# Kernel optimization log

Hardware: AMD Instinct MI355X
Metric: run time of the kernel (lower is better)

The kernel has to match this reference:

```python
import jax, jax.numpy as jnp
import numpy as np

B, T, C, H = 4, 2048, 1024, 16
HS = C // H  # head_size = 64
FF = 4 * C   # 4096
EPS = 1e-5


def _layernorm(x, g, b):
    mu = jnp.mean(x, axis=-1, keepdims=True)
    var = jnp.mean(jnp.square(x - mu), axis=-1, keepdims=True)
    return (x - mu) * jax.lax.rsqrt(var + EPS) * g + b


def setup_inputs() -> dict:
    key = jax.random.key(0)
    ks = jax.random.split(key, 12)
    s_in = 1.0 / np.sqrt(C)
    s_ff = 1.0 / np.sqrt(FF)
    return {
        "x": jax.random.normal(ks[0], (B, T, C), jnp.float32),
        # per-head projection weights stacked: [H, C, HS]
        "Wq": jax.random.normal(ks[1], (H, C, HS), jnp.float32) * s_in,
        "Wk": jax.random.normal(ks[2], (H, C, HS), jnp.float32) * s_in,
        "Wv": jax.random.normal(ks[3], (H, C, HS), jnp.float32) * s_in,
        "Wo": jax.random.normal(ks[4], (C, C), jnp.float32) * s_in,
        "bo": jnp.zeros((C,), jnp.float32),
        "g1": jnp.ones((C,), jnp.float32),
        "b1": jnp.zeros((C,), jnp.float32),
        "g2": jnp.ones((C,), jnp.float32),
        "b2": jnp.zeros((C,), jnp.float32),
        "W1": jax.random.normal(ks[5], (C, FF), jnp.float32) * s_in,
        "bf1": jnp.zeros((FF,), jnp.float32),
        "W2": jax.random.normal(ks[6], (FF, C), jnp.float32) * s_ff,
        "bf2": jnp.zeros((C,), jnp.float32),
    }


def reference(x, Wq, Wk, Wv, Wo, bo, g1, b1, g2, b2, W1, bf1, W2, bf2):
    # pre-norm
    h = _layernorm(x, g1, b1)                       # [B,T,C]
    q = jnp.einsum('btc,hcd->bhtd', h, Wq)          # [B,H,T,HS]
    k = jnp.einsum('btc,hcd->bhtd', h, Wk)
    v = jnp.einsum('btc,hcd->bhtd', h, Wv)
    w = jnp.einsum('bhtd,bhsd->bhts', q, k) * (HS ** -0.5)  # [B,H,T,S]
    mask = jnp.tril(jnp.ones((T, T), bool))          # causal tril
    w = jnp.where(mask[None, None], w, -jnp.inf)
    # NB: original code softmaxes over dim=1 of [B,T,T], i.e. the QUERY axis
    w = jax.nn.softmax(w, axis=-2)
    o = jnp.einsum('bhts,bhsd->bhtd', w, v)          # [B,H,T,HS]
    o = jnp.transpose(o, (0, 2, 1, 3)).reshape(B, T, C)  # concat heads
    x = x + o @ Wo + bo                              # residual 1 (dropout=0)
    f = _layernorm(x, g2, b2)
    ff = jax.nn.relu(f @ W1 + bf1) @ W2 + bf2        # FFN (dropout=0)
    return x + ff
```

## Files before the change

kernel.cpp:

```cpp
#include <hip/hip_runtime.h>
#include <hip/hip_bf16.h>


#define T_SEQ 2048
#define SCALE2 0.1803368801f

typedef __attribute__((ext_vector_type(8))) short short8;
typedef __attribute__((ext_vector_type(4))) float f32x4;

typedef __attribute__((address_space(1))) unsigned int g_u32;
typedef __attribute__((address_space(3))) unsigned int l_u32;

__device__ __forceinline__ unsigned short f2bf(float f) {
  __hip_bfloat16 h = __float2bfloat16(f);
  union { __hip_bfloat16 h; unsigned short u; } x; x.h = h;
  return x.u;
}
__device__ __forceinline__ float bf2f(unsigned short u) {
  union { unsigned u; float f; } x; x.u = (unsigned)u << 16;
  return x.f;
}

__device__ __forceinline__ void g2lds16(const void* g, void* l) {
  __builtin_amdgcn_global_load_lds((g_u32*)g, (l_u32*)l, 16, 0, 0);
}

__device__ __forceinline__ int xcd_swz(int flat, int nwg) {
  if ((nwg & 7) != 0) return flat;
  return (flat & 7) * (nwg >> 3) + (flat >> 3);
}

template <int EPI, int BN>
__global__ __launch_bounds__(512, 2) void gemm256(
    const unsigned short* __restrict__ A, const unsigned short* __restrict__ Bt,
    int M, int N, int K,
    unsigned short* __restrict__ out16, float* __restrict__ outF,
    const float* __restrict__ bias, const float* __restrict__ resid) {
  constexpr int WN = BN / 4;
  constexpr int FN = WN / 16;
  extern __shared__ unsigned short lds[];
  unsigned short* ldsA = lds;
  unsigned short* ldsB = lds + 2 * 16384;
  const int tid = threadIdx.x, lane = tid & 63, wid = tid >> 6;
  const int wm = wid >> 2, wn = wid & 3;
  const int nx = gridDim.x;
  const int flat = blockIdx.y * nx + blockIdx.x;
  const int swz = xcd_swz(flat, nx * gridDim.y);
  const int mBase = (swz / nx) * 256, nBase = (swz % nx) * BN;

  f32x4 acc[8][FN];
#pragma unroll
  for (int i = 0; i < 8; ++i)
#pragma unroll
    for (int j = 0; j < FN; ++j)
#pragma unroll
      for (int e = 0; e < 4; ++e) acc[i][j][e] = 0.f;

  auto stage = [&](int buf, int kt) {
    const int k0 = kt << 6;
#pragma unroll
    for (int it = 0; it < 4; ++it) {
      int g = it * 512 + tid;
      int row = g >> 3, colL = g & 7;
      int col = colL ^ (row & 7);
      g2lds16(A + ((size_t)(mBase + row) * K + k0 + col * 8),
              &ldsA[buf * 16384 + (it * 512 + wid * 64) * 8]);
    }
#pragma unroll
    for (int it = 0; it < (BN * 8) / 512; ++it) {
      int g = it * 512 + tid;
      int row = g >> 3, colL = g & 7;
      int col = colL ^ (row & 7);
      g2lds16(Bt + ((size_t)(nBase + row) * K + k0 + col * 8),
              &ldsB[buf * (BN * 64) + (it * 512 + wid * 64) * 8]);
    }
  };

  const int nKT = K >> 6;
  stage(0, 0);
  __syncthreads();
  int cur = 0;
  for (int kt = 0; kt < nKT; ++kt) {
    if (kt + 1 < nKT) stage(cur ^ 1, kt + 1);

    short8 bf[FN][2];
#pragma unroll
    for (int fn = 0; fn < FN; ++fn)
#pragma unroll
      for (int ks = 0; ks < 2; ++ks) {
        int r = wn * WN + fn * 16 + (lane & 15);
        int c = (ks * 4 + (lane >> 4)) ^ (r & 7);
        bf[fn][ks] = *(const short8*)&ldsB[cur * (BN * 64) + r * 64 + c * 8];
      }
#pragma unroll
    for (int q = 0; q < 4; ++q) {
      short8 af[2][2];
#pragma unroll
      for (int mf = 0; mf < 2; ++mf)
#pragma unroll
        for (int ks = 0; ks < 2; ++ks) {
          int r = wm * 128 + q * 32 + mf * 16 + (lane & 15);
          int c = (ks * 4 + (lane >> 4)) ^ (r & 7);
          af[mf][ks] = *(const short8*)&ldsA[cur * 16384 + r * 64 + c * 8];
        }
      __builtin_amdgcn_s_setprio(1);
#pragma unroll
      for (int mf = 0; mf < 2; ++mf)
#pragma unroll
        for (int fn = 0; fn < FN; ++fn)
#pragma unroll
          for (int ks = 0; ks < 2; ++ks)
            acc[q * 2 + mf][fn] = __builtin_amdgcn_mfma_f32_16x16x32_bf16(
                af[mf][ks], bf[fn][ks], acc[q * 2 + mf][fn], 0, 0, 0);
      __builtin_amdgcn_s_setprio(0);
    }
    __syncthreads();
    cur ^= 1;
  }

#pragma unroll
  for (int am = 0; am < 8; ++am)
#pragma unroll
    for (int fn = 0; fn < FN; ++fn) {
      int col = nBase + wn * WN + fn * 16 + (lane & 15);
      int row0 = mBase + wm * 128 + am * 16 + ((lane >> 4) << 2);
      if (EPI == 0) {
#pragma unroll
        for (int r = 0; r < 4; ++r)
          out16[(size_t)(row0 + r) * N + col] = f2bf(acc[am][fn][r]);
      } else if (EPI == 1) {
        float bv = bias[col];
#pragma unroll
        for (int r = 0; r < 4; ++r) {
          size_t idx = (size_t)(row0 + r) * N + col;
          outF[idx] = acc[am][fn][r] + bv + resid[idx];
        }
      } else {
        float bv = bias[col];
#pragma unroll
        for (int r = 0; r < 4; ++r)
          out16[(size_t)(row0 + r) * N + col] =
              f2bf(fmaxf(acc[am][fn][r] + bv, 0.f));
      }
    }
}

__global__ __launch_bounds__(256) void ln_bf16(
    const float* __restrict__ x, const float* __restrict__ gw,
    const float* __restrict__ bw, unsigned short* __restrict__ out) {
  __shared__ float red[8];
  const int row = blockIdx.x, tid = threadIdx.x;
  const float4 v = ((const float4*)(x + (size_t)row * 1024))[tid];
  float s = v.x + v.y + v.z + v.w;
  float q = v.x * v.x + v.y * v.y + v.z * v.z + v.w * v.w;
#pragma unroll
  for (int off = 32; off >= 1; off >>= 1) {
    s += __shfl_down(s, off);
    q += __shfl_down(q, off);
  }
  const int lane = tid & 63, wid = tid >> 6;
  if (lane == 0) { red[wid] = s; red[4 + wid] = q; }
  __syncthreads();
  float S = red[0] + red[1] + red[2] + red[3];
  float Q = red[4] + red[5] + red[6] + red[7];
  float mu = S * (1.f / 1024.f);
  float var = Q * (1.f / 1024.f) - mu * mu;
  float rs = rsqrtf(var + 1e-5f);
  int c = tid * 4;
  ushort4 ov;
  ov.x = f2bf((v.x - mu) * rs * gw[c + 0] + bw[c + 0]);
  ov.y = f2bf((v.y - mu) * rs * gw[c + 1] + bw[c + 1]);
  ov.z = f2bf((v.z - mu) * rs * gw[c + 2] + bw[c + 2]);
  ov.w = f2bf((v.w - mu) * rs * gw[c + 3] + bw[c + 3]);
  *(ushort4*)&out[(size_t)row * 1024 + c] = ov;
}

__global__ __launch_bounds__(256) void pack_qkv(
    const float* __restrict__ Wq, const float* __restrict__ Wk,
    const float* __restrict__ Wv, unsigned short* __restrict__ out) {
  __shared__ float tile[64 * 65];
  const int tid = threadIdx.x;
  const float* W = (blockIdx.z == 0) ? Wq : (blockIdx.z == 1) ? Wk : Wv;
  const int h = blockIdx.y, r0 = blockIdx.x * 64;
#pragma unroll
  for (int it = 0; it < 4; ++it) {
    int e4 = it * 256 + tid;
    int r = e4 >> 4, c4 = e4 & 15;
    float4 v = *(const float4*)&W[((size_t)h * 1024 + r0 + r) * 64 + c4 * 4];
    tile[r * 65 + c4 * 4 + 0] = v.x;
    tile[r * 65 + c4 * 4 + 1] = v.y;
    tile[r * 65 + c4 * 4 + 2] = v.z;
    tile[r * 65 + c4 * 4 + 3] = v.w;
  }
  __syncthreads();
#pragma unroll
  for (int it = 0; it < 4; ++it) {
    int e4 = it * 256 + tid;
    int d = e4 >> 4, r4 = e4 & 15;
    ushort4 ov;
    ov.x = f2bf(tile[(r4 * 4 + 0) * 65 + d]);
    ov.y = f2bf(tile[(r4 * 4 + 1) * 65 + d]);
    ov.z = f2bf(tile[(r4 * 4 + 2) * 65 + d]);
    ov.w = f2bf(tile[(r4 * 4 + 3) * 65 + d]);
    *(ushort4*)&out[(size_t)(blockIdx.z * 1024 + h * 64 + d) * 1024 + r0 +
                    r4 * 4] = ov;
  }
}

__global__ __launch_bounds__(256) void transpose_cast(
    const float* __restrict__ in, unsigned short* __restrict__ out, int R,
    int C) {
  __shared__ float tile[64 * 65];
  const int tid = threadIdx.x;
  const int r0 = blockIdx.x * 64, c0 = blockIdx.y * 64;
#pragma unroll
  for (int it = 0; it < 4; ++it) {
    int e4 = it * 256 + tid;
    int r = e4 >> 4, c4 = e4 & 15;
    float4 v = *(const float4*)&in[(size_t)(r0 + r) * C + c0 + c4 * 4];
    tile[r * 65 + c4 * 4 + 0] = v.x;
    tile[r * 65 + c4 * 4 + 1] = v.y;
    tile[r * 65 + c4 * 4 + 2] = v.z;
    tile[r * 65 + c4 * 4 + 3] = v.w;
  }
  __syncthreads();
#pragma unroll
  for (int it = 0; it < 4; ++it) {
    int e4 = it * 256 + tid;
    int c = e4 >> 4, r4 = e4 & 15;
    ushort4 ov;
    ov.x = f2bf(tile[(r4 * 4 + 0) * 65 + c]);
    ov.y = f2bf(tile[(r4 * 4 + 1) * 65 + c]);
    ov.z = f2bf(tile[(r4 * 4 + 2) * 65 + c]);
    ov.w = f2bf(tile[(r4 * 4 + 3) * 65 + c]);
    *(ushort4*)&out[(size_t)(c0 + c) * R + r0 + r4 * 4] = ov;
  }
}

__global__ __launch_bounds__(256) void vtrans(
    const unsigned short* __restrict__ qkv, const float* __restrict__ lpart,
    unsigned short* __restrict__ vT) {
  __shared__ unsigned short tile[64 * 66];
  const int tid = threadIdx.x;
  const int bh = blockIdx.y, b = bh >> 4, h = bh & 15;
  const int t0 = blockIdx.x * 64;
#pragma unroll
  for (int it = 0; it < 8; ++it) {
    int e2 = it * 256 + tid;
    int r = e2 >> 5, c2 = e2 & 31;
    unsigned v = *(const unsigned*)&qkv[(size_t)(b * T_SEQ + t0 + r) * 3072 +
                                        2048 + h * 64 + c2 * 2];
    float l0 = lpart[(size_t)bh * T_SEQ + t0 + r];
    float l1 = lpart[(size_t)(64 + bh) * T_SEQ + t0 + r];
    float li = 1.f / (l0 + l1);
    unsigned short lo = f2bf(bf2f((unsigned short)(v & 0xffff)) * li);
    unsigned short hi = f2bf(bf2f((unsigned short)(v >> 16)) * li);
    *(unsigned*)&tile[r * 66 + c2 * 2] = (unsigned)lo | ((unsigned)hi << 16);
  }
  __syncthreads();
#pragma unroll
  for (int it = 0; it < 8; ++it) {
    int e2 = it * 256 + tid;
    int d = e2 >> 5, t2 = e2 & 31;
    unsigned short a = tile[(t2 * 2) * 66 + d];
    unsigned short bb = tile[(t2 * 2 + 1) * 66 + d];
    unsigned pk = (unsigned)a | ((unsigned)bb << 16);
    *(unsigned*)&vT[(size_t)(bh * 64 + d) * T_SEQ + t0 + t2 * 2] = pk;
  }
}

__global__ __launch_bounds__(256, 4) void attn_stats(
    const unsigned short* __restrict__ qkv, float* __restrict__ lpart) {
  __shared__ unsigned short qt[4][2][32 * 64];
  __shared__ float redL[4][2][64];
  const int tid = threadIdx.x, lane = tid & 63, w = tid >> 6;
  const int f = xcd_swz(blockIdx.y * 32 + blockIdx.x, 2048);
  const int half = f & 1, px = (f >> 1) & 15, bh = f >> 5;
  const int b = bh >> 4, h = bh & 15;
  const int sxA = px, sxB = 31 - px;
  const int sA = sxA * 64, sB = sxB * 64;
  const int m = half * 4 + w;

  short8 kfA[4][2], kfB[4][2];
#pragma unroll
  for (int fn = 0; fn < 4; ++fn)
#pragma unroll
    for (int ks = 0; ks < 2; ++ks) {
      int d = 1024 + h * 64 + ks * 32 + ((lane >> 4) << 3);
      kfA[fn][ks] = *(const short8*)&qkv[(size_t)(b * T_SEQ + sA + fn * 16 +
                                                  (lane & 15)) * 3072 + d];
      kfB[fn][ks] = *(const short8*)&qkv[(size_t)(b * T_SEQ + sB + fn * 16 +
                                                  (lane & 15)) * 3072 + d];
    }
  float lA[4] = {0.f, 0.f, 0.f, 0.f}, lB[4] = {0.f, 0.f, 0.f, 0.f};

  auto stageQ = [&](int buf, int idx) {
    int t0 = idx * 32;
#pragma unroll
    for (int it = 0; it < 4; ++it) {
      int g = it * 64 + lane;
      int row = g >> 3;
      int col = (g & 7) ^ (row & 7);
      g2lds16(qkv + ((size_t)(b * T_SEQ + t0 + row) * 3072 + h * 64 + col * 8),
              &qt[w][buf][it * 512]);
    }
  };

  auto accum = [&](const short8 (&af)[2], const short8 (&kf)[4][2],
                   float (&lacc)[4], int sBase, int tRow, bool diag) {
    f32x4 sc[4];
#pragma unroll
    for (int fn = 0; fn < 4; ++fn)
#pragma unroll
      for (int e = 0; e < 4; ++e) sc[fn][e] = 0.f;
    __builtin_amdgcn_s_setprio(1);
#pragma unroll
    for (int fn = 0; fn < 4; ++fn)
#pragma unroll
      for (int ks = 0; ks < 2; ++ks)
        sc[fn] = __builtin_amdgcn_mfma_f32_16x16x32_bf16(af[ks], kf[fn][ks],
                                                         sc[fn], 0, 0, 0);
    __builtin_amdgcn_s_setprio(0);
    if (diag) {
#pragma unroll
      for (int fn = 0; fn < 4; ++fn) {
        int s = sBase + fn * 16 + (lane & 15);
        float e0 = (tRow + 0 >= s) ? exp2f(sc[fn][0] * SCALE2) : 0.f;
        float e1 = (tRow + 1 >= s) ? exp2f(sc[fn][1] * SCALE2) : 0.f;
        float e2 = (tRow + 2 >= s) ? exp2f(sc[fn][2] * SCALE2) : 0.f;
        float e3 = (tRow + 3 >= s) ? exp2f(sc[fn][3] * SCALE2) : 0.f;
        lacc[fn] += (e0 + e1) + (e2 + e3);
      }
    } else {
#pragma unroll
      for (int fn = 0; fn < 4; ++fn) {
        float e0 = exp2f(sc[fn][0] * SCALE2);
        float e1 = exp2f(sc[fn][1] * SCALE2);
        float e2 = exp2f(sc[fn][2] * SCALE2);
        float e3 = exp2f(sc[fn][3] * SCALE2);
        lacc[fn] += (e0 + e1) + (e2 + e3);
      }
    }
  };

  const int d0 = 2 * sxA - m;
  const int fi = m + (d0 > 0 ? (((d0 + 7) >> 3) << 3) : 0);
  int cur = 0;
  if (fi < 64) stageQ(0, fi);
  for (int idx = fi; idx < 64; idx += 8, cur ^= 1) {
    if (idx + 8 < 64) {
      stageQ(cur ^ 1, idx + 8);
      asm volatile("s_waitcnt vmcnt(4)" ::: "memory");
    } else {
      asm volatile("s_waitcnt vmcnt(0)" ::: "memory");
    }
    const int t0g = idx * 32;
    const bool doB = idx >= 2 * sxB;
#pragma unroll
    for (int mf = 0; mf < 2; ++mf) {
      short8 af[2];
#pragma unroll
      for (int ks = 0; ks < 2; ++ks) {
        int r = mf * 16 + (lane & 15);
        int c = (ks * 4 + (lane >> 4)) ^ (r & 7);
        af[ks] = *(const short8*)&qt[w][cur][r * 64 + c * 8];
      }
      int tRow = t0g + mf * 16 + ((lane >> 4) << 2);
      accum(af, kfA, lA, sA, tRow, idx <= 2 * sxA + 1);
      if (doB) accum(af, kfB, lB, sB, tRow, idx <= 2 * sxB + 1);
    }
  }
#pragma unroll
  for (int fn = 0; fn < 4; ++fn) {
    lA[fn] += __shfl_down(lA[fn], 32);
    lA[fn] += __shfl_down(lA[fn], 16);
    lB[fn] += __shfl_down(lB[fn], 32);
    lB[fn] += __shfl_down(lB[fn], 16);
  }
  if (lane < 16) {
#pragma unroll
    for (int fn = 0; fn < 4; ++fn) {
      redL[w][0][fn * 16 + lane] = lA[fn];
      redL[w][1][fn * 16 + lane] = lB[fn];
    }
  }
  __syncthreads();
  if (tid < 128) {
    int which = tid >> 6;
    float l = redL[0][which][lane] + redL[1][which][lane] +
              redL[2][which][lane] + redL[3][which][lane];
    int sbase = (which == 0) ? sA : sB;
    lpart[((size_t)half * 64 + bh) * T_SEQ + sbase + lane] = l;
  }
}

__global__ __launch_bounds__(256, 2) void attn_pv(
    const unsigned short* __restrict__ qkv, const unsigned short* __restrict__ vT,
    unsigned short* __restrict__ o) {
  __shared__ unsigned short kbuf[2][64 * 64];
  __shared__ unsigned short vbuf[2][64 * 64];
  __shared__ unsigned short pl[256 * 64];
  const int tid = threadIdx.x, lane = tid & 63, wid = tid >> 6;
  const int f = xcd_swz(blockIdx.y * 8 + blockIdx.x, 512);
  const int bx = f & 7, bh = f >> 3;
  const int b = bh >> 4, h = bh & 15;
  const int tA = bx * 128, tB = (15 - bx) * 128;
  const int nSTA = 2 * bx + 2, nSTB = 32 - 2 * bx;

  short8 qfA[2][2], qfB[2][2];
#pragma unroll
  for (int mf = 0; mf < 2; ++mf)
#pragma unroll
    for (int ks = 0; ks < 2; ++ks) {
      int d = h * 64 + ks * 32 + ((lane >> 4) << 3);
      int rloc = wid * 32 + mf * 16 + (lane & 15);
      qfA[mf][ks] =
          *(const short8*)&qkv[(size_t)(b * T_SEQ + tA + rloc) * 3072 + d];
      qfB[mf][ks] =
          *(const short8*)&qkv[(size_t)(b * T_SEQ + tB + rloc) * 3072 + d];
    }
  f32x4 oaccA[2][4], oaccB[2][4];
#pragma unroll
  for (int i = 0; i < 2; ++i)
#pragma unroll
    for (int j = 0; j < 4; ++j)
#pragma unroll
      for (int e = 0; e < 4; ++e) { oaccA[i][j][e] = 0.f; oaccB[i][j][e] = 0.f; }

  auto stage = [&](int buf, int st) {
#pragma unroll
    for (int it = 0; it < 2; ++it) {
      int g = it * 256 + tid;
      int row = g >> 3, colL = g & 7;
      int col = colL ^ (row & 7);
      g2lds16(qkv + ((size_t)(b * T_SEQ + st * 64 + row) * 3072 + 1024 +
                     h * 64 + col * 8),
              &kbuf[buf][(it * 256 + wid * 64) * 8]);
      g2lds16(vT + ((size_t)(bh * 64 + row) * T_SEQ + st * 64 + col * 8),
              &vbuf[buf][(it * 256 + wid * 64) * 8]);
    }
  };

  auto qkstore = [&](const short8 (&qf)[2][2], int rowBase, int tBase, int s0,
                     bool maskNeeded, int cur) {
    f32x4 sc[2][4];
#pragma unroll
    for (int i = 0; i < 2; ++i)
#pragma unroll
      for (int j = 0; j < 4; ++j)
#pragma unroll
        for (int e = 0; e < 4; ++e) sc[i][j][e] = 0.f;
    __builtin_amdgcn_s_setprio(1);
#pragma unroll
    for (int fn = 0; fn < 4; ++fn)
#pragma unroll
      for (int ks = 0; ks < 2; ++ks) {
        int r = fn * 16 + (lane & 15);
        int c = (ks * 4 + (lane >> 4)) ^ (r & 7);
        short8 kfr = *(const short8*)&kbuf[cur][r * 64 + c * 8];
        sc[0][fn] = __builtin_amdgcn_mfma_f32_16x16x32_bf16(qf[0][ks], kfr,
                                                            sc[0][fn], 0, 0, 0);
        sc[1][fn] = __builtin_amdgcn_mfma_f32_16x16x32_bf16(qf[1][ks], kfr,
                                                            sc[1][fn], 0, 0, 0);
      }
    __builtin_amdgcn_s_setprio(0);
#pragma unroll
    for (int fn = 0; fn < 4; ++fn) {
      int sg = s0 + fn * 16 + (lane & 15);
      int colb = (fn * 16 + (lane & 15)) * 2;
#pragma unroll
      for (int mf = 0; mf < 2; ++mf) {
        int rowB = rowBase + wid * 32 + mf * 16 + ((lane >> 4) << 2);
        int tRow = tBase + wid * 32 + mf * 16 + ((lane >> 4) << 2);
#pragma unroll
        for (int r = 0; r < 4; ++r) {
          float p = exp2f(sc[mf][fn][r] * SCALE2);
          if (maskNeeded) p = (tRow + r >= sg) ? p : 0.f;
          int row = rowB + r;
          int byteoff = row * 128 + (colb ^ ((row & 7) << 4));
          *(unsigned short*)((char*)pl + byteoff) = f2bf(p);
        }
      }
    }
  };

  stage(0, 0);
  int cur = 0;
  __syncthreads();

  for (int st = 0; st < nSTB; ++st) {
    const int s0 = st * 64;
    const bool doA = st < nSTA;

    if (doA) qkstore(qfA, 0, tA, s0, st >= nSTA - 2, cur);
    qkstore(qfB, 128, tB, s0, st >= nSTB - 2, cur);
    __syncthreads();

    if (st + 1 < nSTB) stage(cur ^ 1, st + 1);

    __builtin_amdgcn_s_setprio(1);
#pragma unroll
    for (int ks = 0; ks < 2; ++ks) {
      short8 paA[2], paB[2];
#pragma unroll
      for (int mf = 0; mf < 2; ++mf) {
        int rowa = wid * 32 + mf * 16 + (lane & 15);
        int kb = ks * 64 + ((lane >> 4) << 4);
        paB[mf] = *(const short8*)((const char*)pl + (128 + rowa) * 128 +
                                   (kb ^ ((rowa & 7) << 4)));
        if (doA)
          paA[mf] = *(const short8*)((const char*)pl + rowa * 128 +
                                     (kb ^ ((rowa & 7) << 4)));
      }
#pragma unroll
      for (int df = 0; df < 4; ++df) {
        int r = df * 16 + (lane & 15);
        int c = (ks * 4 + (lane >> 4)) ^ (r & 7);
        short8 vb = *(const short8*)&vbuf[cur][r * 64 + c * 8];
        oaccB[0][df] = __builtin_amdgcn_mfma_f32_16x16x32_bf16(paB[0], vb,
                                                               oaccB[0][df], 0, 0, 0);
        oaccB[1][df] = __builtin_amdgcn_mfma_f32_16x16x32_bf16(paB[1], vb,
                                                               oaccB[1][df], 0, 0, 0);
        if (doA) {
          oaccA[0][df] = __builtin_amdgcn_mfma_f32_16x16x32_bf16(paA[0], vb,
                                                                 oaccA[0][df], 0, 0, 0);
          oaccA[1][df] = __builtin_amdgcn_mfma_f32_16x16x32_bf16(paA[1], vb,
                                                                 oaccA[1][df], 0, 0, 0);
        }
      }
    }
    __builtin_amdgcn_s_setprio(0);
    __syncthreads();
    cur ^= 1;
  }
#pragma unroll
  for (int mf = 0; mf < 2; ++mf)
#pragma unroll
    for (int df = 0; df < 4; ++df) {
      int d = h * 64 + df * 16 + (lane & 15);
      int ra = tA + wid * 32 + mf * 16 + ((lane >> 4) << 2);
      int rb = tB + wid * 32 + mf * 16 + ((lane >> 4) << 2);
#pragma unroll
      for (int r = 0; r < 4; ++r) {
        o[(size_t)(b * T_SEQ + ra + r) * 1024 + d] = f2bf(oaccA[mf][df][r]);
        o[(size_t)(b * T_SEQ + rb + r) * 1024 + d] = f2bf(oaccB[mf][df][r]);
      }
    }
}

extern "C" void kernel_launch(void* const* d_in, const int* in_sizes, int n_in,
                              void* d_out, int out_size, void* d_ws,
                              size_t ws_size, hipStream_t stream) {
  const float* x = (const float*)d_in[0];
  const float* Wq = (const float*)d_in[1];
  const float* Wk = (const float*)d_in[2];
  const float* Wv = (const float*)d_in[3];
  const float* Wo = (const float*)d_in[4];
  const float* bo = (const float*)d_in[5];
  const float* g1 = (const float*)d_in[6];
  const float* b1 = (const float*)d_in[7];
  const float* g2 = (const float*)d_in[8];
  const float* b2 = (const float*)d_in[9];
  const float* W1 = (const float*)d_in[10];
  const float* bf1 = (const float*)d_in[11];
  const float* W2 = (const float*)d_in[12];
  const float* bf2 = (const float*)d_in[13];
  float* out = (float*)d_out;

  char* ws = (char*)d_ws;
  size_t off = 0;
  auto alloc = [&](size_t bytes) {
    char* p = ws + off;
    off += (bytes + 255) & ~(size_t)255;
    return p;
  };
  unsigned short* Wqkv = (unsigned short*)alloc(3072ull * 1024 * 2);
  unsigned short* WoT = (unsigned short*)alloc(1024ull * 1024 * 2);
  unsigned short* W1T = (unsigned short*)alloc(4096ull * 1024 * 2);
  unsigned short* W2T = (unsigned short*)alloc(1024ull * 4096 * 2);
  unsigned short* hbuf = (unsigned short*)alloc(8192ull * 1024 * 2);
  char* regionE = alloc(8192ull * 3072 * 2 + 64ull * 64 * 2048 * 2);
  unsigned short* qkv = (unsigned short*)regionE;
  unsigned short* vT = (unsigned short*)(regionE + 8192ull * 3072 * 2);
  unsigned short* act = (unsigned short*)regionE;
  float* lbuf = (float*)alloc(128ull * 2048 * 4);
  float* x1 = (float*)alloc(8192ull * 1024 * 4);
  unsigned short* fbuf = (unsigned short*)alloc(8192ull * 1024 * 2);
  unsigned short* obuf = hbuf;

  (void)in_sizes; (void)n_in; (void)out_size; (void)ws_size;

  const size_t LDS128 = (2 * 16384 + 2 * 128 * 64) * 2;
  const size_t LDS256 = (2 * 16384 + 2 * 256 * 64) * 2;

  pack_qkv<<<dim3(16, 16, 3), 256, 0, stream>>>(Wq, Wk, Wv, Wqkv);
  transpose_cast<<<dim3(16, 16), 256, 0, stream>>>(Wo, WoT, 1024, 1024);
  transpose_cast<<<dim3(16, 64), 256, 0, stream>>>(W1, W1T, 1024, 4096);
  transpose_cast<<<dim3(64, 16), 256, 0, stream>>>(W2, W2T, 4096, 1024);
  ln_bf16<<<8192, 256, 0, stream>>>(x, g1, b1, hbuf);
  gemm256<0, 128><<<dim3(24, 32), 512, LDS128, stream>>>(
      hbuf, Wqkv, 8192, 3072, 1024, qkv, nullptr, nullptr, nullptr);
  attn_stats<<<dim3(32, 64), 256, 0, stream>>>(qkv, lbuf);
  vtrans<<<dim3(32, 64), 256, 0, stream>>>(qkv, lbuf, vT);
  attn_pv<<<dim3(8, 64), 256, 0, stream>>>(qkv, vT, obuf);
  gemm256<1, 128><<<dim3(8, 32), 512, LDS128, stream>>>(
      obuf, WoT, 8192, 1024, 1024, nullptr, x1, bo, x);
  ln_bf16<<<8192, 256, 0, stream>>>(x1, g2, b2, fbuf);
  gemm256<2, 256><<<dim3(16, 32), 512, LDS256, stream>>>(
      fbuf, W1T, 8192, 4096, 1024, act, nullptr, bf1, nullptr);
  gemm256<1, 128><<<dim3(8, 32), 512, LDS128, stream>>>(
      act, W2T, 8192, 1024, 4096, nullptr, out, bf2, x1);
}
```

Measured before the change: 437.6 us.

## Halve P tile LDS in attn_pv and serialize A/B phases for occupancy

Shrinks the shared P buffer from 256 to 128 rows by processing the A and B query tiles one after another, each with its own QK-store and PV phase. Raises launch bounds from 2 to 3 blocks per CU. Issues the next K/V stage before compute and replaces __syncthreads with explicit waitcnt plus s_barrier. The aim is more resident blocks and earlier prefetch, at the cost of extra barriers per iteration and tighter register limits that may cause spills.

```diff
diff --git a/kernel.cpp b/kernel.cpp
--- a/kernel.cpp
+++ b/kernel.cpp
@@ -394,12 +394,12 @@
   }
 }
 
-__global__ __launch_bounds__(256, 2) void attn_pv(
+__global__ __launch_bounds__(256, 3) void attn_pv(
     const unsigned short* __restrict__ qkv, const unsigned short* __restrict__ vT,
     unsigned short* __restrict__ o) {
   __shared__ unsigned short kbuf[2][64 * 64];
   __shared__ unsigned short vbuf[2][64 * 64];
-  __shared__ unsigned short pl[256 * 64];
+  __shared__ unsigned short pl[128 * 64];
   const int tid = threadIdx.x, lane = tid & 63, wid = tid >> 6;
   const int f = xcd_swz(blockIdx.y * 8 + blockIdx.x, 512);
   const int bx = f & 7, bh = f >> 3;
@@ -441,7 +441,7 @@
     }
   };
 
-  auto qkstore = [&](const short8 (&qf)[2][2], int rowBase, int tBase, int s0,
+  auto qkstore = [&](const short8 (&qf)[2][2], int tBase, int s0,
                      bool maskNeeded, int cur) {
     f32x4 sc[2][4];
 #pragma unroll
@@ -470,7 +470,7 @@
       int colb = (fn * 16 + (lane & 15)) * 2;
 #pragma unroll
       for (int mf = 0; mf < 2; ++mf) {
-        int rowB = rowBase + wid * 32 + mf * 16 + ((lane >> 4) << 2);
+        int rowB = wid * 32 + mf * 16 + ((lane >> 4) << 2);
         int tRow = tBase + wid * 32 + mf * 16 + ((lane >> 4) << 2);
 #pragma unroll
         for (int r = 0; r < 4; ++r) {
@@ -484,53 +484,65 @@
     }
   };
 
-  stage(0, 0);
-  int cur = 0;
-  __syncthreads();
-
-  for (int st = 0; st < nSTB; ++st) {
-    const int s0 = st * 64;
-    const bool doA = st < nSTA;
-
-    if (doA) qkstore(qfA, 0, tA, s0, st >= nSTA - 2, cur);
-    qkstore(qfB, 128, tB, s0, st >= nSTB - 2, cur);
-    __syncthreads();
-
-    if (st + 1 < nSTB) stage(cur ^ 1, st + 1);
-
+  auto pvphase = [&](f32x4 (&oacc)[2][4], int cur) {
     __builtin_amdgcn_s_setprio(1);
 #pragma unroll
     for (int ks = 0; ks < 2; ++ks) {
-      short8 paA[2], paB[2];
+      short8 pa[2];
 #pragma unroll
       for (int mf = 0; mf < 2; ++mf) {
         int rowa = wid * 32 + mf * 16 + (lane & 15);
         int kb = ks * 64 + ((lane >> 4) << 4);
-        paB[mf] = *(const short8*)((const char*)pl + (128 + rowa) * 128 +
-                                   (kb ^ ((rowa & 7) << 4)));
-        if (doA)
-          paA[mf] = *(const short8*)((const char*)pl + rowa * 128 +
-                                     (kb ^ ((rowa & 7) << 4)));
+        pa[mf] = *(const short8*)((const char*)pl + rowa * 128 +
+                                  (kb ^ ((rowa & 7) << 4)));
       }
 #pragma unroll
       for (int df = 0; df < 4; ++df) {
         int r = df * 16 + (lane & 15);
         int c = (ks * 4 + (lane >> 4)) ^ (r & 7);
         short8 vb = *(const short8*)&vbuf[cur][r * 64 + c * 8];
-        oaccB[0][df] = __builtin_amdgcn_mfma_f32_16x16x32_bf16(paB[0], vb,
-                                                               oaccB[0][df], 0, 0, 0);
-        oaccB[1][df] = __builtin_amdgcn_mfma_f32_16x16x32_bf16(paB[1], vb,
-                                                               oaccB[1][df], 0, 0, 0);
-        if (doA) {
-          oaccA[0][df] = __builtin_amdgcn_mfma_f32_16x16x32_bf16(paA[0], vb,
-                                                                 oaccA[0][df], 0, 0, 0);
-          oaccA[1][df] = __builtin_amdgcn_mfma_f32_16x16x32_bf16(paA[1], vb,
-                                                                 oaccA[1][df], 0, 0, 0);
-        }
+        oacc[0][df] = __builtin_amdgcn_mfma_f32_16x16x32_bf16(pa[0], vb,
+                                                              oacc[0][df], 0, 0, 0);
+        oacc[1][df] = __builtin_amdgcn_mfma_f32_16x16x32_bf16(pa[1], vb,
+                                                              oacc[1][df], 0, 0, 0);
       }
     }
     __builtin_amdgcn_s_setprio(0);
-    __syncthreads();
+  };
+
+  auto bar_lgkm = [&]() {
+    asm volatile("s_waitcnt lgkmcnt(0)" ::: "memory");
+    __builtin_amdgcn_sched_barrier(0);
+    __builtin_amdgcn_s_barrier();
+    __builtin_amdgcn_sched_barrier(0);
+  };
+
+  stage(0, 0);
+  asm volatile("s_waitcnt vmcnt(0)" ::: "memory");
+  __builtin_amdgcn_sched_barrier(0);
+  __builtin_amdgcn_s_barrier();
+  __builtin_amdgcn_sched_barrier(0);
+
+  int cur = 0;
+  for (int st = 0; st < nSTB; ++st) {
+    const int s0 = st * 64;
+    const bool doA = st < nSTA;
+
+    if (st + 1 < nSTB) stage(cur ^ 1, st + 1);
+
+    if (doA) {
+      qkstore(qfA, tA, s0, st >= nSTA - 2, cur);
+      bar_lgkm();
+      pvphase(oaccA, cur);
+      bar_lgkm();
+    }
+    qkstore(qfB, tB, s0, st >= nSTB - 2, cur);
+    bar_lgkm();
+    pvphase(oaccB, cur);
+    asm volatile("s_waitcnt vmcnt(0) lgkmcnt(0)" ::: "memory");
+    __builtin_amdgcn_sched_barrier(0);
+    __builtin_amdgcn_s_barrier();
+    __builtin_amdgcn_sched_barrier(0);
     cur ^= 1;
   }
 #pragma unroll
```

Measured after the change: 524.1 us. +19.8%, slower.
